# Kernel tuning notes

Measured on AMD Instinct MI355X. Metric: run time of the kernel, lower is better.

Reference implementation:

```python
import jax, jax.numpy as jnp
import numpy as np

N_NODES = 50000
N_EDGES = 1600000
D = 128


def setup_inputs() -> dict:
    key = jax.random.key(0)
    ks = jax.random.split(key, 8)
    features = jax.random.normal(ks[0], (N_NODES, D), dtype=jnp.float32)
    edge_src = jax.random.randint(ks[1], (N_EDGES,), 0, N_NODES, dtype=jnp.int32)
    edge_dst = jax.random.randint(ks[2], (N_EDGES,), 0, N_NODES, dtype=jnp.int32)
    edge_weight = jax.random.uniform(ks[3], (N_EDGES,), dtype=jnp.float32)
    scale = 1.0 / np.sqrt(D)
    W1 = jax.random.normal(ks[4], (D, D), dtype=jnp.float32) * scale
    b1 = jnp.zeros((D,), dtype=jnp.float32)
    W2 = jax.random.normal(ks[5], (D, D), dtype=jnp.float32) * scale
    b2 = jnp.zeros((D,), dtype=jnp.float32)
    return {"features": features, "edge_src": edge_src, "edge_dst": edge_dst,
            "edge_weight": edge_weight, "W1": W1, "b1": b1, "W2": W2, "b2": b2}


def _gcn_layer(x, W, b, edge_src, edge_dst, edge_weight, n_nodes):
    # support = X @ W  (dense projection), then spmm: out[d] += w_e * support[s]
    support = x @ W  # [N, D]
    msgs = support[edge_src] * edge_weight[:, None]  # [E, D] gather + scale
    out = jax.ops.segment_sum(msgs, edge_dst, num_segments=n_nodes)  # scatter-add
    return out + b


def reference(features, edge_src, edge_dst, edge_weight, W1, b1, W2, b2):
    h = _gcn_layer(features, W1, b1, edge_src, edge_dst, edge_weight, N_NODES)
    h = jax.nn.relu(h)
    # dropout is identity in eval mode (training=False)
    out = _gcn_layer(h, W2, b2, edge_src, edge_dst, edge_weight, N_NODES)
    return out
```

## Files before the change

kernel.cpp:

```cpp
#include <hip/hip_runtime.h>
#include <hip/hip_fp16.h>
#include <math.h>

#define D 128
#define BSHIFT 7
#define BSIZE (1 << BSHIFT)
#define CHUNK 8192
#define BT 1024
#define CAP 7168
#define LDP 136
#define SENTV 0xFFFFFFFFu

typedef _Float16 half8 __attribute__((ext_vector_type(8)));
typedef float f32x4 __attribute__((ext_vector_type(4)));
typedef float f32x2 __attribute__((ext_vector_type(2)));

#if __has_builtin(__builtin_amdgcn_cvt_pk_f32_fp8) && \
    __has_builtin(__builtin_amdgcn_cvt_pk_fp8_f32)
#define HAVE_FP8_CVT 1
#endif

__device__ __forceinline__ float dec_e4m3(unsigned int b) {
    const unsigned int e = (b >> 3) & 0xF;
    const unsigned int m = b & 7;
    float v;
    if (e == 0) v = (float)m * 0.001953125f;
    else        v = (float)(8 + m) * __uint_as_float((e + 117) << 23);
    return (b & 0x80) ? -v : v;
}

__device__ __forceinline__ unsigned char enc_fp8(float x) {
#ifdef HAVE_FP8_CVT
    return (unsigned char)(__builtin_amdgcn_cvt_pk_fp8_f32(x, x, 0, false) & 0xFF);
#else
    const float ax0 = fabsf(x);
    const unsigned int s = (x < 0.f) ? 0x80u : 0u;
    const float ax = fminf(ax0, 448.0f);
    if (ax < 0.015625f) {
        const int m = __float2int_rn(ax * 512.0f);
        return (unsigned char)(s | (unsigned int)m);
    }
    int ex;
    const float fr = frexpf(ax, &ex);
    int m = __float2int_rn(fr * 16.0f) - 8;
    int e = ex - 1 + 7;
    if (m == 8) { m = 0; e += 1; }
    if (e > 15) return (unsigned char)(s | 0x7E);
    return (unsigned char)(s | ((unsigned int)e << 3) | (unsigned int)m);
#endif
}

__global__ __launch_bounds__(512) void init_bcur(int* __restrict__ bcur, int NB) {
    const int b = blockIdx.x * 512 + threadIdx.x;
    if (b < NB) bcur[b] = b * CAP;
}

__device__ __forceinline__ void gemm_body_f32(const float* __restrict__ X,
                                              const __half* __restrict__ Wt,
                                              unsigned char* __restrict__ Y,
                                              int M, int bx) {
    const int lane = threadIdx.x & 63;
    const int wv = threadIdx.x >> 6;
    const int row0 = bx * 256 + wv * 16;
    const int m = lane & 15;
    const int q = lane >> 4;

    if (row0 >= M) return;
    const int rsafe = min(row0 + m, M - 1);
    const float4* Xr = (const float4*)(X + (size_t)rsafe * D);
    half8 a[4];
#pragma unroll
    for (int kt = 0; kt < 4; ++kt) {
        const float4 lo = Xr[kt * 8 + q * 2];
        const float4 hi = Xr[kt * 8 + q * 2 + 1];
        a[kt] = (half8){(_Float16)lo.x, (_Float16)lo.y, (_Float16)lo.z,
                        (_Float16)lo.w, (_Float16)hi.x, (_Float16)hi.y,
                        (_Float16)hi.z, (_Float16)hi.w};
    }

    const half8* WT8 = (const half8*)Wt;
#pragma unroll
    for (int ct = 0; ct < 8; ++ct) {
        const int n = ct * 16 + m;
        f32x4 acc = {0.f, 0.f, 0.f, 0.f};
#pragma unroll
        for (int kt = 0; kt < 4; ++kt) {
            const half8 b = WT8[(size_t)n * 16 + kt * 4 + q];
            acc = __builtin_amdgcn_mfma_f32_16x16x32_f16(a[kt], b, acc, 0, 0, 0);
        }
#pragma unroll
        for (int r = 0; r < 4; ++r) {
            const int orow = row0 + q * 4 + r;
            if (orow < M)
                Y[(size_t)orow * D + ct * 16 + m] = enc_fp8(acc[r]);
        }
    }
}

__global__ __launch_bounds__(BT) void scatter_prep(const int* __restrict__ src,
                                                   const int* __restrict__ dst,
                                                   const float* __restrict__ wgt,
                                                   int* __restrict__ bcur,
                                                   unsigned int* __restrict__ csrA,
                                                   int E, int NB, int nscat,
                                                   const float* __restrict__ W1,
                                                   const float* __restrict__ W2,
                                                   __half* __restrict__ W1t,
                                                   __half* __restrict__ W2t) {
    if (blockIdx.x >= (unsigned)nscat) {
        const int which = blockIdx.x - nscat;
        const float* W = which ? W2 : W1;
        __half* Wt = which ? W2t : W1t;
        for (int i = threadIdx.x; i < D * D; i += BT) {
            const int n = i >> 7, k = i & 127;
            Wt[i] = __float2half(W[k * D + n]);
        }
        return;
    }

    __shared__ int lhist[512];
    __shared__ int lstart[512];
    __shared__ int lcur[512];
    const int tid = threadIdx.x;
    const int base = blockIdx.x * CHUNK;

    for (int b = tid; b < NB; b += BT) lhist[b] = 0;
    __syncthreads();

    int dreg[CHUNK / BT];
#pragma unroll
    for (int u = 0; u < CHUNK / BT; ++u) {
        const int e = base + u * BT + tid;
        dreg[u] = (e < E) ? dst[e] : -1;
        if (dreg[u] >= 0) atomicAdd(&lhist[dreg[u] >> BSHIFT], 1);
    }
    __syncthreads();

    for (int b = tid; b < NB; b += BT) {
        const int c = lhist[b];
        if (c) {
            const int r = atomicAdd(&bcur[b], (c + 15) & ~15);
            lstart[b] = r;
            lcur[b] = r;
        }
    }
    __syncthreads();

#pragma unroll
    for (int u = 0; u < CHUNK / BT; ++u) {
        const int d = dreg[u];
        if (d >= 0) {
            const int e = base + u * BT + tid;
            const int b = d >> BSHIFT;
            const int pos = atomicAdd(&lcur[b], 1);
            const unsigned int wq =
                (unsigned int)__float2int_rn(wgt[e] * 511.0f);
            const unsigned int kv = (unsigned int)src[e] |
                                    ((unsigned int)(d & (BSIZE - 1)) << 16) |
                                    (wq << 23);
            if (pos < (b + 1) * CAP) csrA[pos] = kv;
        }
    }
    __syncthreads();

    for (int b = tid; b < NB; b += BT) {
        const int c = lhist[b];
        if (c) {
            const int beg = lstart[b] + c;
            const int fin = lstart[b] + ((c + 15) & ~15);
            for (int p = beg; p < fin; ++p)
                if (p < (b + 1) * CAP) csrA[p] = SENTV;
        }
    }
}

__global__ __launch_bounds__(BT) void sort_gemm1(const unsigned int* __restrict__ csrA,
                                                 const int* __restrict__ bcur,
                                                 int* __restrict__ offsets,
                                                 int* __restrict__ deg,
                                                 unsigned int* __restrict__ csr,
                                                 int M, int NB,
                                                 const float* __restrict__ X,
                                                 const __half* __restrict__ W1t,
                                                 unsigned char* __restrict__ sup) {
    if (blockIdx.x >= (unsigned)NB) {
        gemm_body_f32(X, W1t, sup, M, blockIdx.x - NB);
        return;
    }

    __shared__ int hist[BSIZE];
    __shared__ int ncur[BSIZE];
    __shared__ int wtot[2];
    const int b = blockIdx.x;
    const int n0 = b << BSHIFT;
    const int tid = threadIdx.x;
    const int nloc = min(BSIZE, M - n0);
    const int bstart = b * CAP;
    const int bend = min(bcur[b], (b + 1) * CAP);

    if (tid < BSIZE) hist[tid] = 0;
    __syncthreads();

    unsigned int reg[CAP / BT];
#pragma unroll
    for (int i = 0; i < CAP / BT; ++i) {
        const int j = bstart + i * BT + tid;
        unsigned int kv = SENTV;
        if (j < bend) kv = csrA[j];
        reg[i] = kv;
        if ((kv & 0xFFFFu) != 0xFFFFu)
            atomicAdd(&hist[(kv >> 16) & (BSIZE - 1)], 1);
    }
    __syncthreads();

    const int lane = tid & 63;
    const int wv = tid >> 6;
    const int v = (tid < BSIZE) ? hist[tid] : 0;
    int incl = v;
#pragma unroll
    for (int off = 1; off < 64; off <<= 1) {
        int t = __shfl_up(incl, off, 64);
        if (lane >= off) incl += t;
    }
    if (tid < BSIZE && lane == 63) wtot[wv] = incl;
    __syncthreads();
    const int carry = (wv == 1) ? wtot[0] : 0;
    const int excl = bstart + incl - v + carry;
    if (tid < nloc) {
        offsets[n0 + tid] = excl;
        deg[n0 + tid] = v;
        ncur[tid] = excl;
    }
    __syncthreads();

#pragma unroll
    for (int i = 0; i < CAP / BT; ++i) {
        const unsigned int kv = reg[i];
        if ((kv & 0xFFFFu) != 0xFFFFu) {
            const int pos = atomicAdd(&ncur[(kv >> 16) & (BSIZE - 1)], 1);
            csr[pos] = kv;
        }
    }
}

__device__ __forceinline__ void accum8(float acc[8], uint2 raw, float w) {
#ifdef HAVE_FP8_CVT
    const f32x2 f01 = __builtin_amdgcn_cvt_pk_f32_fp8(raw.x, false);
    const f32x2 f23 = __builtin_amdgcn_cvt_pk_f32_fp8(raw.x, true);
    const f32x2 f45 = __builtin_amdgcn_cvt_pk_f32_fp8(raw.y, false);
    const f32x2 f67 = __builtin_amdgcn_cvt_pk_f32_fp8(raw.y, true);
    acc[0] = fmaf(w, f01[0], acc[0]);
    acc[1] = fmaf(w, f01[1], acc[1]);
    acc[2] = fmaf(w, f23[0], acc[2]);
    acc[3] = fmaf(w, f23[1], acc[3]);
    acc[4] = fmaf(w, f45[0], acc[4]);
    acc[5] = fmaf(w, f45[1], acc[5]);
    acc[6] = fmaf(w, f67[0], acc[6]);
    acc[7] = fmaf(w, f67[1], acc[7]);
#else
#pragma unroll
    for (int i = 0; i < 4; ++i)
        acc[i] = fmaf(w, dec_e4m3((raw.x >> (8 * i)) & 0xFF), acc[i]);
#pragma unroll
    for (int i = 0; i < 4; ++i)
        acc[4 + i] = fmaf(w, dec_e4m3((raw.y >> (8 * i)) & 0xFF), acc[4 + i]);
#endif
}

__device__ __forceinline__ float kv_w(unsigned int kv) {
    return (float)(kv >> 23) * (1.0f / 511.0f);
}

__device__ __forceinline__ void gather_row(const uint2* __restrict__ supv,
                                           const unsigned int* __restrict__ csr,
                                           int beg, int end, int l, float acc[8]) {
    int j = beg;
    for (; j + 16 <= end; j += 16) {
        unsigned int kv[16];
        uint2 r[16];
#pragma unroll
        for (int u = 0; u < 16; ++u) kv[u] = csr[j + u];
#pragma unroll
        for (int u = 0; u < 16; ++u)
            r[u] = supv[(size_t)(kv[u] & 0xFFFF) * 16 + l];
#pragma unroll
        for (int u = 0; u < 16; ++u) accum8(acc, r[u], kv_w(kv[u]));
    }
    if (j + 8 <= end) {
        unsigned int kv[8];
        uint2 r[8];
#pragma unroll
        for (int u = 0; u < 8; ++u) kv[u] = csr[j + u];
#pragma unroll
        for (int u = 0; u < 8; ++u)
            r[u] = supv[(size_t)(kv[u] & 0xFFFF) * 16 + l];
#pragma unroll
        for (int u = 0; u < 8; ++u) accum8(acc, r[u], kv_w(kv[u]));
        j += 8;
    }
    if (j + 4 <= end) {
        unsigned int kv[4];
        uint2 r[4];
#pragma unroll
        for (int u = 0; u < 4; ++u) kv[u] = csr[j + u];
#pragma unroll
        for (int u = 0; u < 4; ++u)
            r[u] = supv[(size_t)(kv[u] & 0xFFFF) * 16 + l];
#pragma unroll
        for (int u = 0; u < 4; ++u) accum8(acc, r[u], kv_w(kv[u]));
        j += 4;
    }
    for (; j < end; ++j) {
        const unsigned int kv = csr[j];
        const uint2 r = supv[(size_t)(kv & 0xFFFF) * 16 + l];
        accum8(acc, r, kv_w(kv));
    }
}

__global__ __launch_bounds__(256) void gather_gemm(const unsigned char* __restrict__ sup,
                                                   const int* __restrict__ offsets,
                                                   const int* __restrict__ deg,
                                                   const unsigned int* __restrict__ csr,
                                                   const float* __restrict__ b1,
                                                   const __half* __restrict__ W2t,
                                                   unsigned char* __restrict__ sup2,
                                                   int M) {
    __shared__ _Float16 hA[16 * LDP];
    const int tid = threadIdx.x;
    const int q = tid >> 4;
    const int l = tid & 15;
    const int n = blockIdx.x * 16 + q;

    float acc[8];
    {
        const float4 c0 = ((const float4*)b1)[l * 2];
        const float4 c1 = ((const float4*)b1)[l * 2 + 1];
        acc[0] = c0.x; acc[1] = c0.y; acc[2] = c0.z; acc[3] = c0.w;
        acc[4] = c1.x; acc[5] = c1.y; acc[6] = c1.z; acc[7] = c1.w;
    }
    if (n < M) {
        const int beg = offsets[n];
        gather_row((const uint2*)sup, csr, beg, beg + deg[n], l, acc);
    }

    half8 hv;
#pragma unroll
    for (int i = 0; i < 8; ++i) hv[i] = (_Float16)fmaxf(acc[i], 0.f);
    *(half8*)&hA[q * LDP + l * 8] = hv;
    __syncthreads();

    const int lane = tid & 63;
    const int wv = tid >> 6;
    const int m = lane & 15;
    const int qq = lane >> 4;
    half8 a[4];
#pragma unroll
    for (int kt = 0; kt < 4; ++kt)
        a[kt] = *(const half8*)&hA[m * LDP + kt * 32 + qq * 8];

    const half8* WT8 = (const half8*)W2t;
#pragma unroll
    for (int c = 0; c < 2; ++c) {
        const int ct = wv * 2 + c;
        const int ncol = ct * 16 + m;
        f32x4 dacc = {0.f, 0.f, 0.f, 0.f};
#pragma unroll
        for (int kt = 0; kt < 4; ++kt) {
            const half8 b = WT8[(size_t)ncol * 16 + kt * 4 + qq];
            dacc = __builtin_amdgcn_mfma_f32_16x16x32_f16(a[kt], b, dacc, 0, 0, 0);
        }
#pragma unroll
        for (int r = 0; r < 4; ++r) {
            const int orow = blockIdx.x * 16 + qq * 4 + r;
            if (orow < M)
                sup2[(size_t)orow * D + ct * 16 + m] = enc_fp8(dacc[r]);
        }
    }
}

__global__ __launch_bounds__(256) void gather_out(const unsigned char* __restrict__ sup,
                                                  const int* __restrict__ offsets,
                                                  const int* __restrict__ deg,
                                                  const unsigned int* __restrict__ csr,
                                                  const float* __restrict__ bias,
                                                  float* __restrict__ out, int M) {
    const int tid = threadIdx.x;
    const int q = tid >> 4;
    const int l = tid & 15;
    const int n = blockIdx.x * 16 + q;
    if (n >= M) return;

    float acc[8];
    {
        const float4 c0 = ((const float4*)bias)[l * 2];
        const float4 c1 = ((const float4*)bias)[l * 2 + 1];
        acc[0] = c0.x; acc[1] = c0.y; acc[2] = c0.z; acc[3] = c0.w;
        acc[4] = c1.x; acc[5] = c1.y; acc[6] = c1.z; acc[7] = c1.w;
    }
    const int beg = offsets[n];
    gather_row((const uint2*)sup, csr, beg, beg + deg[n], l, acc);

    f32x4* out4 = (f32x4*)out;
    const f32x4 o0 = {acc[0], acc[1], acc[2], acc[3]};
    const f32x4 o1 = {acc[4], acc[5], acc[6], acc[7]};
    __builtin_nontemporal_store(o0, out4 + (size_t)n * 32 + l * 2);
    __builtin_nontemporal_store(o1, out4 + (size_t)n * 32 + l * 2 + 1);
}

extern "C" void kernel_launch(void* const* d_in, const int* in_sizes, int n_in,
                              void* d_out, int out_size, void* d_ws, size_t ws_size,
                              hipStream_t stream) {
    const float* features = (const float*)d_in[0];
    const int*   esrc     = (const int*)d_in[1];
    const int*   edst     = (const int*)d_in[2];
    const float* ew       = (const float*)d_in[3];
    const float* W1       = (const float*)d_in[4];
    const float* b1       = (const float*)d_in[5];
    const float* W2       = (const float*)d_in[6];
    const float* b2       = (const float*)d_in[7];
    float* out = (float*)d_out;

    const int M = in_sizes[0] / D;
    const int E = in_sizes[1];
    const int NB = (M + BSIZE - 1) >> BSHIFT;

    unsigned int* csrA = (unsigned int*)d_ws;
    unsigned int* csr  = csrA + (size_t)NB * CAP;
    unsigned char* sup = (unsigned char*)(csr + (size_t)NB * CAP);
    unsigned char* sup2 = sup + (size_t)M * D;
    int*    offsets = (int*)(sup2 + (size_t)M * D);
    int*    deg     = offsets + M;
    int*    bcur    = deg + M;
    __half* W1t     = (__half*)(bcur + NB);
    __half* W2t     = W1t + D * D;

    const int gemm_blocks = (M + 255) / 256;
    const int node_blocks = (M + 15) / 16;
    const int nscat = (E + CHUNK - 1) / CHUNK;

    init_bcur<<<1, 512, 0, stream>>>(bcur, NB);
    scatter_prep<<<nscat + 2, BT, 0, stream>>>(esrc, edst, ew, bcur, csrA, E, NB,
                                               nscat, W1, W2, W1t, W2t);
    sort_gemm1<<<NB + gemm_blocks, BT, 0, stream>>>(csrA, bcur, offsets, deg, csr,
                                                    M, NB, features, W1t, sup);
    gather_gemm<<<node_blocks, 256, 0, stream>>>(sup, offsets, deg, csr, b1, W2t,
                                                 sup2, M);
    gather_out<<<node_blocks, 256, 0, stream>>>(sup2, offsets, deg, csr, b2, out, M);
}
```

Measured before the change: 212.0 us.

## Split feature tables into column slices and unfuse gather from second GEMM

Stores the fp8 support matrices as four column slices of 32 bytes per node, so each gather block works on a single slice. Each slice is 50000×32 B, about 1.6 MB, small enough to stay cache-resident during the random row gathers. The first gather no longer runs the W2 projection in the same kernel. It writes ReLU'd activations as fp8 in the sliced layout, and a separate gemm2 kernel reads them back. In exchange it adds one kernel launch and an extra round-trip through memory, re-reads the CSR once per slice, and quantizes the hidden activations to fp8 where they were fp16 before.

New measurement: 236.1 us. 11.4% more time.

```diff
diff --git a/kernel.cpp b/kernel.cpp
--- a/kernel.cpp
+++ b/kernel.cpp
@@ -8,8 +8,9 @@
 #define CHUNK 8192
 #define BT 1024
 #define CAP 7168
-#define LDP 136
 #define SENTV 0xFFFFFFFFu
+#define NSL 4
+#define SLW 32
 
 typedef _Float16 half8 __attribute__((ext_vector_type(8)));
 typedef float f32x4 __attribute__((ext_vector_type(4)));
@@ -50,6 +51,22 @@
 #endif
 }
 
+__device__ __forceinline__ void dec8(uint2 v, float f[8]) {
+#ifdef HAVE_FP8_CVT
+    const f32x2 f01 = __builtin_amdgcn_cvt_pk_f32_fp8(v.x, false);
+    const f32x2 f23 = __builtin_amdgcn_cvt_pk_f32_fp8(v.x, true);
+    const f32x2 f45 = __builtin_amdgcn_cvt_pk_f32_fp8(v.y, false);
+    const f32x2 f67 = __builtin_amdgcn_cvt_pk_f32_fp8(v.y, true);
+    f[0] = f01[0]; f[1] = f01[1]; f[2] = f23[0]; f[3] = f23[1];
+    f[4] = f45[0]; f[5] = f45[1]; f[6] = f67[0]; f[7] = f67[1];
+#else
+#pragma unroll
+    for (int i = 0; i < 4; ++i) f[i] = dec_e4m3((v.x >> (8 * i)) & 0xFF);
+#pragma unroll
+    for (int i = 0; i < 4; ++i) f[4 + i] = dec_e4m3((v.y >> (8 * i)) & 0xFF);
+#endif
+}
+
 __global__ __launch_bounds__(512) void init_bcur(int* __restrict__ bcur, int NB) {
     const int b = blockIdx.x * 512 + threadIdx.x;
     if (b < NB) bcur[b] = b * CAP;
@@ -92,7 +109,8 @@
         for (int r = 0; r < 4; ++r) {
             const int orow = row0 + q * 4 + r;
             if (orow < M)
-                Y[(size_t)orow * D + ct * 16 + m] = enc_fp8(acc[r]);
+                Y[(size_t)(ct >> 1) * M * SLW + (size_t)orow * SLW +
+                  (ct & 1) * 16 + m] = enc_fp8(acc[r]);
         }
     }
 }
@@ -243,37 +261,20 @@
     }
 }
 
-__device__ __forceinline__ void accum8(float acc[8], uint2 raw, float w) {
-#ifdef HAVE_FP8_CVT
-    const f32x2 f01 = __builtin_amdgcn_cvt_pk_f32_fp8(raw.x, false);
-    const f32x2 f23 = __builtin_amdgcn_cvt_pk_f32_fp8(raw.x, true);
-    const f32x2 f45 = __builtin_amdgcn_cvt_pk_f32_fp8(raw.y, false);
-    const f32x2 f67 = __builtin_amdgcn_cvt_pk_f32_fp8(raw.y, true);
-    acc[0] = fmaf(w, f01[0], acc[0]);
-    acc[1] = fmaf(w, f01[1], acc[1]);
-    acc[2] = fmaf(w, f23[0], acc[2]);
-    acc[3] = fmaf(w, f23[1], acc[3]);
-    acc[4] = fmaf(w, f45[0], acc[4]);
-    acc[5] = fmaf(w, f45[1], acc[5]);
-    acc[6] = fmaf(w, f67[0], acc[6]);
-    acc[7] = fmaf(w, f67[1], acc[7]);
-#else
-#pragma unroll
-    for (int i = 0; i < 4; ++i)
-        acc[i] = fmaf(w, dec_e4m3((raw.x >> (8 * i)) & 0xFF), acc[i]);
-#pragma unroll
-    for (int i = 0; i < 4; ++i)
-        acc[4 + i] = fmaf(w, dec_e4m3((raw.y >> (8 * i)) & 0xFF), acc[4 + i]);
-#endif
-}
-
 __device__ __forceinline__ float kv_w(unsigned int kv) {
     return (float)(kv >> 23) * (1.0f / 511.0f);
 }
 
-__device__ __forceinline__ void gather_row(const uint2* __restrict__ supv,
-                                           const unsigned int* __restrict__ csr,
-                                           int beg, int end, int l, float acc[8]) {
+__device__ __forceinline__ void accum8(float acc[8], uint2 raw, float w) {
+    float f[8];
+    dec8(raw, f);
+#pragma unroll
+    for (int i = 0; i < 8; ++i) acc[i] = fmaf(w, f[i], acc[i]);
+}
+
+__device__ __forceinline__ void gather_row_sl(const uint2* __restrict__ supv,
+                                              const unsigned int* __restrict__ csr,
+                                              int beg, int end, int p, float acc[8]) {
     int j = beg;
     for (; j + 16 <= end; j += 16) {
         unsigned int kv[16];
@@ -282,7 +283,7 @@
         for (int u = 0; u < 16; ++u) kv[u] = csr[j + u];
 #pragma unroll
         for (int u = 0; u < 16; ++u)
-            r[u] = supv[(size_t)(kv[u] & 0xFFFF) * 16 + l];
+            r[u] = supv[(size_t)(kv[u] & 0xFFFF) * 4 + p];
 #pragma unroll
         for (int u = 0; u < 16; ++u) accum8(acc, r[u], kv_w(kv[u]));
     }
@@ -293,7 +294,7 @@
         for (int u = 0; u < 8; ++u) kv[u] = csr[j + u];
 #pragma unroll
         for (int u = 0; u < 8; ++u)
-            r[u] = supv[(size_t)(kv[u] & 0xFFFF) * 16 + l];
+            r[u] = supv[(size_t)(kv[u] & 0xFFFF) * 4 + p];
 #pragma unroll
         for (int u = 0; u < 8; ++u) accum8(acc, r[u], kv_w(kv[u]));
         j += 8;
@@ -305,106 +306,121 @@
         for (int u = 0; u < 4; ++u) kv[u] = csr[j + u];
 #pragma unroll
         for (int u = 0; u < 4; ++u)
-            r[u] = supv[(size_t)(kv[u] & 0xFFFF) * 16 + l];
+            r[u] = supv[(size_t)(kv[u] & 0xFFFF) * 4 + p];
 #pragma unroll
         for (int u = 0; u < 4; ++u) accum8(acc, r[u], kv_w(kv[u]));
         j += 4;
     }
     for (; j < end; ++j) {
         const unsigned int kv = csr[j];
-        const uint2 r = supv[(size_t)(kv & 0xFFFF) * 16 + l];
-        accum8(acc, r, kv_w(kv));
-    }
-}
-
-__global__ __launch_bounds__(256) void gather_gemm(const unsigned char* __restrict__ sup,
-                                                   const int* __restrict__ offsets,
-                                                   const int* __restrict__ deg,
-                                                   const unsigned int* __restrict__ csr,
-                                                   const float* __restrict__ b1,
-                                                   const __half* __restrict__ W2t,
-                                                   unsigned char* __restrict__ sup2,
-                                                   int M) {
-    __shared__ _Float16 hA[16 * LDP];
+        accum8(acc, supv[(size_t)(kv & 0xFFFF) * 4 + p], kv_w(kv));
+    }
+}
+
+__global__ __launch_bounds__(256) void gather1_sl(const unsigned char* __restrict__ sup,
+                                                  const int* __restrict__ offsets,
+                                                  const int* __restrict__ deg,
+                                                  const unsigned int* __restrict__ csr,
+                                                  const float* __restrict__ b1,
+                                                  unsigned char* __restrict__ h,
+                                                  int M) {
+    const int sl = blockIdx.x & (NSL - 1);
+    const int nb = blockIdx.x >> 2;
     const int tid = threadIdx.x;
-    const int q = tid >> 4;
-    const int l = tid & 15;
-    const int n = blockIdx.x * 16 + q;
+    const int g = tid >> 2;
+    const int p = tid & 3;
+    const int n = nb * 64 + g;
+    if (n >= M) return;
 
     float acc[8];
     {
-        const float4 c0 = ((const float4*)b1)[l * 2];
-        const float4 c1 = ((const float4*)b1)[l * 2 + 1];
+        const float4 c0 = ((const float4*)b1)[sl * 8 + p * 2];
+        const float4 c1 = ((const float4*)b1)[sl * 8 + p * 2 + 1];
         acc[0] = c0.x; acc[1] = c0.y; acc[2] = c0.z; acc[3] = c0.w;
         acc[4] = c1.x; acc[5] = c1.y; acc[6] = c1.z; acc[7] = c1.w;
     }
-    if (n < M) {
-        const int beg = offsets[n];
-        gather_row((const uint2*)sup, csr, beg, beg + deg[n], l, acc);
-    }
-
-    half8 hv;
-#pragma unroll
-    for (int i = 0; i < 8; ++i) hv[i] = (_Float16)fmaxf(acc[i], 0.f);
-    *(half8*)&hA[q * LDP + l * 8] = hv;
-    __syncthreads();
-
-    const int lane = tid & 63;
-    const int wv = tid >> 6;
+    const uint2* supv = (const uint2*)(sup + (size_t)sl * M * SLW);
+    const int beg = offsets[n];
+    gather_row_sl(supv, csr, beg, beg + deg[n], p, acc);
+
+    unsigned char* hr = h + (size_t)sl * M * SLW + (size_t)n * SLW + p * 8;
+#pragma unroll
+    for (int i = 0; i < 8; ++i) hr[i] = enc_fp8(fmaxf(acc[i], 0.f));
+}
+
+__global__ __launch_bounds__(256) void gemm2(const unsigned char* __restrict__ h,
+                                             const __half* __restrict__ W2t,
+                                             unsigned char* __restrict__ sup2, int M) {
+    const int lane = threadIdx.x & 63;
+    const int wv = threadIdx.x >> 6;
+    const int row0 = blockIdx.x * 64 + wv * 16;
     const int m = lane & 15;
-    const int qq = lane >> 4;
+    const int q = lane >> 4;
+
+    if (row0 >= M) return;
+    const int rsafe = min(row0 + m, M - 1);
     half8 a[4];
 #pragma unroll
-    for (int kt = 0; kt < 4; ++kt)
-        a[kt] = *(const half8*)&hA[m * LDP + kt * 32 + qq * 8];
+    for (int kt = 0; kt < 4; ++kt) {
+        const uint2 v = *(const uint2*)(h + (size_t)kt * M * SLW +
+                                        (size_t)rsafe * SLW + q * 8);
+        float f[8];
+        dec8(v, f);
+        a[kt] = (half8){(_Float16)f[0], (_Float16)f[1], (_Float16)f[2],
+                        (_Float16)f[3], (_Float16)f[4], (_Float16)f[5],
+                        (_Float16)f[6], (_Float16)f[7]};
+    }
 
     const half8* WT8 = (const half8*)W2t;
 #pragma unroll
-    for (int c = 0; c < 2; ++c) {
-        const int ct = wv * 2 + c;
-        const int ncol = ct * 16 + m;
-        f32x4 dacc = {0.f, 0.f, 0.f, 0.f};
+    for (int ct = 0; ct < 8; ++ct) {
+        const int n = ct * 16 + m;
+        f32x4 acc = {0.f, 0.f, 0.f, 0.f};
 #pragma unroll
         for (int kt = 0; kt < 4; ++kt) {
-            const half8 b = WT8[(size_t)ncol * 16 + kt * 4 + qq];
-            dacc = __builtin_amdgcn_mfma_f32_16x16x32_f16(a[kt], b, dacc, 0, 0, 0);
+            const half8 b = WT8[(size_t)n * 16 + kt * 4 + q];
+            acc = __builtin_amdgcn_mfma_f32_16x16x32_f16(a[kt], b, acc, 0, 0, 0);
         }
 #pragma unroll
         for (int r = 0; r < 4; ++r) {
-            const int orow = blockIdx.x * 16 + qq * 4 + r;
+            const int orow = row0 + q * 4 + r;
             if (orow < M)
-                sup2[(size_t)orow * D + ct * 16 + m] = enc_fp8(dacc[r]);
-        }
-    }
-}
-
-__global__ __launch_bounds__(256) void gather_out(const unsigned char* __restrict__ sup,
+                sup2[(size_t)(ct >> 1) * M * SLW + (size_t)orow * SLW +
+                     (ct & 1) * 16 + m] = enc_fp8(acc[r]);
+        }
+    }
+}
+
+__global__ __launch_bounds__(256) void gather2_sl(const unsigned char* __restrict__ sup,
                                                   const int* __restrict__ offsets,
                                                   const int* __restrict__ deg,
                                                   const unsigned int* __restrict__ csr,
                                                   const float* __restrict__ bias,
                                                   float* __restrict__ out, int M) {
+    const int sl = blockIdx.x & (NSL - 1);
+    const int nb = blockIdx.x >> 2;
     const int tid = threadIdx.x;
-    const int q = tid >> 4;
-    const int l = tid & 15;
-    const int n = blockIdx.x * 16 + q;
+    const int g = tid >> 2;
+    const int p = tid & 3;
+    const int n = nb * 64 + g;
     if (n >= M) return;
 
     float acc[8];
     {
-        const float4 c0 = ((const float4*)bias)[l * 2];
-        const float4 c1 = ((const float4*)bias)[l * 2 + 1];
+        const float4 c0 = ((const float4*)bias)[sl * 8 + p * 2];
+        const float4 c1 = ((const float4*)bias)[sl * 8 + p * 2 + 1];
         acc[0] = c0.x; acc[1] = c0.y; acc[2] = c0.z; acc[3] = c0.w;
         acc[4] = c1.x; acc[5] = c1.y; acc[6] = c1.z; acc[7] = c1.w;
     }
+    const uint2* supv = (const uint2*)(sup + (size_t)sl * M * SLW);
     const int beg = offsets[n];
-    gather_row((const uint2*)sup, csr, beg, beg + deg[n], l, acc);
-
-    f32x4* out4 = (f32x4*)out;
+    gather_row_sl(supv, csr, beg, beg + deg[n], p, acc);
+
+    f32x4* out4 = (f32x4*)(out + (size_t)n * D + sl * SLW + p * 8);
     const f32x4 o0 = {acc[0], acc[1], acc[2], acc[3]};
     const f32x4 o1 = {acc[4], acc[5], acc[6], acc[7]};
-    __builtin_nontemporal_store(o0, out4 + (size_t)n * 32 + l * 2);
-    __builtin_nontemporal_store(o1, out4 + (size_t)n * 32 + l * 2 + 1);
+    __builtin_nontemporal_store(o0, out4);
+    __builtin_nontemporal_store(o1, out4 + 1);
 }
 
 extern "C" void kernel_launch(void* const* d_in, const int* in_sizes, int n_in,
@@ -427,7 +443,8 @@
     unsigned int* csrA = (unsigned int*)d_ws;
     unsigned int* csr  = csrA + (size_t)NB * CAP;
     unsigned char* sup = (unsigned char*)(csr + (size_t)NB * CAP);
-    unsigned char* sup2 = sup + (size_t)M * D;
+    unsigned char* h   = sup + (size_t)M * D;
+    unsigned char* sup2 = h + (size_t)M * D;
     int*    offsets = (int*)(sup2 + (size_t)M * D);
     int*    deg     = offsets + M;
     int*    bcur    = deg + M;
@@ -435,7 +452,7 @@
     __half* W2t     = W1t + D * D;
 
     const int gemm_blocks = (M + 255) / 256;
-    const int node_blocks = (M + 15) / 16;
+    const int nb64 = (M + 63) / 64;
     const int nscat = (E + CHUNK - 1) / CHUNK;
 
     init_bcur<<<1, 512, 0, stream>>>(bcur, NB);
@@ -443,7 +460,7 @@
                                                nscat, W1, W2, W1t, W2t);
     sort_gemm1<<<NB + gemm_blocks, BT, 0, stream>>>(csrA, bcur, offsets, deg, csr,
                                                     M, NB, features, W1t, sup);
-    gather_gemm<<<node_blocks, 256, 0, stream>>>(sup, offsets, deg, csr, b1, W2t,
-                                                 sup2, M);
-    gather_out<<<node_blocks, 256, 0, stream>>>(sup2, offsets, deg, csr, b2, out, M);
-}
+    gather1_sl<<<NSL * nb64, 256, 0, stream>>>(sup, offsets, deg, csr, b1, h, M);
+    gemm2<<<nb64, 256, 0, stream>>>(h, W2t, sup2, M);
+    gather2_sl<<<NSL * nb64, 256, 0, stream>>>(sup2, offsets, deg, csr, b2, out, M);
+}
```
